# Kernel tuning notes

Measured on AMD Instinct MI355X. Metric: run time of the kernel, lower is better.

The kernel has to match this reference:

```python
import jax, jax.numpy as jnp
import numpy as np

FEAT_DIM = 2048
HID = 256
N = 1024
NUM_CLASSES = 16
BN_EPS = 1e-5


def _batchnorm(x, gamma, beta):
    # training-mode BatchNorm1d: per-batch mean, biased variance
    m = x.mean(axis=0)
    v = x.var(axis=0)
    return gamma * (x - m) / jnp.sqrt(v + BN_EPS) + beta


def setup_inputs() -> dict:
    key = jax.random.key(0)
    ks = jax.random.split(key, 12)
    s1 = 1.0 / np.sqrt(FEAT_DIM)
    s2 = 1.0 / np.sqrt(HID)
    s3 = 1.0 / np.sqrt(2 * HID)
    return {
        "features": jax.random.normal(ks[0], (N, FEAT_DIM), dtype=jnp.float32),
        "labels": jax.random.randint(ks[1], (N,), 0, NUM_CLASSES, dtype=jnp.int32),
        # semantic disentangler
        "W1": jax.random.normal(ks[2], (FEAT_DIM, HID), dtype=jnp.float32) * s1,
        "b1": jnp.zeros((HID,), jnp.float32),
        "g1": jnp.ones((HID,), jnp.float32),
        "bt1": jnp.zeros((HID,), jnp.float32),
        "W2": jax.random.normal(ks[3], (HID, HID), dtype=jnp.float32) * s2,
        "b2": jnp.zeros((HID,), jnp.float32),
        "g2": jnp.ones((HID,), jnp.float32),
        "bt2": jnp.zeros((HID,), jnp.float32),
        # edge network: Linear(2H -> H), Linear(H -> 1)
        "We1": jax.random.normal(ks[4], (2 * HID, HID), dtype=jnp.float32) * s3,
        "bwe1": jnp.zeros((HID,), jnp.float32),
        "We2": jax.random.normal(ks[5], (HID, 1), dtype=jnp.float32) * s2,
        "bwe2": jnp.zeros((1,), jnp.float32),
    }


def reference(features, labels, W1, b1, g1, bt1, W2, b2, g2, bt2,
              We1, bwe1, We2, bwe2):
    # semantic disentangler: (Linear -> BN -> ReLU) x2
    h = jax.nn.relu(_batchnorm(features @ W1 + b1, g1, bt1))
    di = jax.nn.relu(_batchnorm(h @ W2 + b2, g2, bt2))  # [N, H]

    # EdgeNetwork all-pairs: Linear on concat([f_i, f_j]) splits into two GEMMs
    hi = di @ We1[:HID]   # [N, H] contribution of node i (first half of concat)
    hj = di @ We1[HID:]   # [N, H] contribution of node j (second half)
    pair = jax.nn.relu(hi[:, None, :] + hj[None, :, :] + bwe1)  # [N, N, H]
    logits = pair @ We2[:, 0] + bwe2[0]                          # [N, N]
    same_label = labels[:, None] == labels[None, :]
    off_diag = ~jnp.eye(N, dtype=bool)
    edge_weights = jnp.where(same_label & off_diag,
                             jax.nn.sigmoid(logits), 0.0)        # [N, N]

    # update_node_features: f_i + sum_j w_ij f_j / sum_j w_ij (if wsum > 0)
    weighted_sum = edge_weights @ di                 # [N, H] (w_ii == 0)
    wsum = edge_weights.sum(axis=1, keepdims=True)   # [N, 1]
    denom = jnp.where(wsum > 0, wsum, 1.0)
    updated = di + jnp.where(wsum > 0, weighted_sum / denom, 0.0)
    return updated
```

## Files before the change

kernel.cpp:

```cpp
#include <hip/hip_runtime.h>
#include <math.h>

#define N_PTS 1024
#define HID   256
#define FEAT  2048

typedef short bf16x8 __attribute__((ext_vector_type(8)));
typedef float f32x4  __attribute__((ext_vector_type(4)));

__device__ inline ushort f2bf(float f) {
    union { float f; unsigned u; } v; v.f = f;
    unsigned r = v.u + 0x7fff + ((v.u >> 16) & 1);
    return (ushort)(r >> 16);
}

__global__ __launch_bounds__(256) void gemm_mfma(
    const float* __restrict__ A, const float* __restrict__ B,
    float* __restrict__ C, int lda, int ldb, int ldc, int kchunk)
{
    __shared__ ushort As[64 * 72];
    __shared__ ushort Bs[64 * 72];
    const int tid  = threadIdx.x;
    const int lane = tid & 63;
    const int wave = tid >> 6;
    const int wy = wave >> 1, wx = wave & 1;
    const int quad = lane >> 4, l16 = lane & 15;
    const int mBase = blockIdx.y * 64;
    const int nBase = blockIdx.x * 64;
    const int kBeg  = blockIdx.z * kchunk;

    f32x4 acc[2][2] = {};

    for (int ks = kBeg; ks < kBeg + kchunk; ks += 64) {
        #pragma unroll
        for (int p = 0; p < 4; p++) {
            const int c  = p * 256 + tid;
            const int r  = c >> 4;
            const int cq = c & 15;
            float4 av = *(const float4*)&A[(size_t)(mBase + r) * lda + ks + cq * 4];
            ushort4 ao;
            ao.x = f2bf(av.x); ao.y = f2bf(av.y);
            ao.z = f2bf(av.z); ao.w = f2bf(av.w);
            *(ushort4*)&As[r * 72 + cq * 4] = ao;
            float4 bv = *(const float4*)&B[(size_t)(ks + r) * ldb + nBase + cq * 4];
            Bs[(cq * 4 + 0) * 72 + r] = f2bf(bv.x);
            Bs[(cq * 4 + 1) * 72 + r] = f2bf(bv.y);
            Bs[(cq * 4 + 2) * 72 + r] = f2bf(bv.z);
            Bs[(cq * 4 + 3) * 72 + r] = f2bf(bv.w);
        }
        __syncthreads();
        #pragma unroll
        for (int kt = 0; kt < 64; kt += 32) {
            bf16x8 af[2], bfr[2];
            #pragma unroll
            for (int mi = 0; mi < 2; mi++)
                af[mi] = *(bf16x8*)&As[(wy * 32 + mi * 16 + l16) * 72 + kt + quad * 8];
            #pragma unroll
            for (int ni = 0; ni < 2; ni++)
                bfr[ni] = *(bf16x8*)&Bs[(wx * 32 + ni * 16 + l16) * 72 + kt + quad * 8];
            #pragma unroll
            for (int mi = 0; mi < 2; mi++)
                #pragma unroll
                for (int ni = 0; ni < 2; ni++)
                    acc[mi][ni] = __builtin_amdgcn_mfma_f32_16x16x32_bf16(
                        af[mi], bfr[ni], acc[mi][ni], 0, 0, 0);
        }
        __syncthreads();
    }
    #pragma unroll
    for (int mi = 0; mi < 2; mi++)
        #pragma unroll
        for (int ni = 0; ni < 2; ni++)
            #pragma unroll
            for (int e = 0; e < 4; e++) {
                const int gm = mBase + wy * 32 + mi * 16 + quad * 4 + e;
                const int gn = nBase + wx * 32 + ni * 16 + l16;
                unsafeAtomicAdd(&C[(size_t)gm * ldc + gn], acc[mi][ni][e]);
            }
}

__global__ __launch_bounds__(256) void colstats(
    const float* __restrict__ X, float* __restrict__ sum,
    float* __restrict__ sq, int rowsPerBlock)
{
    const int c = threadIdx.x;
    const int r0 = blockIdx.x * rowsPerBlock;
    float s = 0.f, q = 0.f;
    for (int r = r0; r < r0 + rowsPerBlock; ++r) {
        float v = X[r * HID + c];
        s += v;
        q = fmaf(v, v, q);
    }
    unsafeAtomicAdd(&sum[c], s);
    unsafeAtomicAdd(&sq[c], q);
}

__global__ __launch_bounds__(256) void bn_relu(
    const float* __restrict__ X, const float* __restrict__ sum,
    const float* __restrict__ sq, const float* __restrict__ g,
    const float* __restrict__ bt, float* __restrict__ Y)
{
    const int idx = blockIdx.x * 256 + threadIdx.x;
    const int cq = (idx & 63) * 4;
    float4 x = ((const float4*)X)[idx];
    float xv[4] = {x.x, x.y, x.z, x.w};
    float o[4];
    #pragma unroll
    for (int e = 0; e < 4; e++) {
        const int c = cq + e;
        float m   = sum[c] * (1.f / 1024.f);
        float var = fmaf(-m, m, sq[c] * (1.f / 1024.f));
        float rstd = rsqrtf(var + 1e-5f);
        o[e] = fmaxf(fmaf(g[c] * rstd, xv[e] - m, bt[c]), 0.f);
    }
    ((float4*)Y)[idx] = make_float4(o[0], o[1], o[2], o[3]);
}

__global__ __launch_bounds__(256) void pair_update(
    const float* __restrict__ di, const float* __restrict__ hi,
    const float* __restrict__ hj, const float* __restrict__ bwe1,
    const float* __restrict__ We2, const float* __restrict__ bwe2,
    const int* __restrict__ labels, float* __restrict__ out)
{
    __shared__ int   slab[N_PTS];
    __shared__ float sacc[4][HID];
    __shared__ float swsum[4];
    const int i = blockIdx.x;
    const int tid = threadIdx.x;
    const int lane = tid & 63;
    const int wave = tid >> 6;

    for (int t = tid; t < N_PTS; t += 256) slab[t] = labels[t];
    __syncthreads();

    const int myLab = slab[i];
    float4 hv_i = ((const float4*)(hi + (size_t)i * HID))[lane];
    float4 bw   = ((const float4*)bwe1)[lane];
    float4 w2   = ((const float4*)We2)[lane];
    const float hb0 = hv_i.x + bw.x, hb1 = hv_i.y + bw.y;
    const float hb2 = hv_i.z + bw.z, hb3 = hv_i.w + bw.w;
    const float b2 = bwe2[0];

    float a0 = 0.f, a1 = 0.f, a2 = 0.f, a3 = 0.f, wsum = 0.f;

    for (int chunk = wave * 64; chunk < N_PTS; chunk += 256) {
        const int j = chunk + lane;
        const bool match = (slab[j] == myLab) && (j != i);
        unsigned long long mask = __ballot(match);
        while (mask) {
            const int bpos = __builtin_ctzll(mask);
            mask &= mask - 1;
            const int jj = chunk + bpos;
            float4 hv = ((const float4*)(hj + (size_t)jj * HID))[lane];
            float p = fmaxf(hb0 + hv.x, 0.f) * w2.x
                    + fmaxf(hb1 + hv.y, 0.f) * w2.y
                    + fmaxf(hb2 + hv.z, 0.f) * w2.z
                    + fmaxf(hb3 + hv.w, 0.f) * w2.w;
            #pragma unroll
            for (int off = 1; off < 64; off <<= 1) p += __shfl_xor(p, off, 64);
            const float w = 1.f / (1.f + expf(-(p + b2)));
            float4 dv = ((const float4*)(di + (size_t)jj * HID))[lane];
            a0 = fmaf(w, dv.x, a0);
            a1 = fmaf(w, dv.y, a1);
            a2 = fmaf(w, dv.z, a2);
            a3 = fmaf(w, dv.w, a3);
            wsum += w;
        }
    }
    ((float4*)sacc[wave])[lane] = make_float4(a0, a1, a2, a3);
    if (lane == 0) swsum[wave] = wsum;
    __syncthreads();

    const float at = sacc[0][tid] + sacc[1][tid] + sacc[2][tid] + sacc[3][tid];
    const float wt = swsum[0] + swsum[1] + swsum[2] + swsum[3];
    const float dval = di[(size_t)i * HID + tid];
    out[(size_t)i * HID + tid] = dval + (wt > 0.f ? at / wt : 0.f);
}

extern "C" void kernel_launch(void* const* d_in, const int* in_sizes, int n_in,
                              void* d_out, int out_size, void* d_ws, size_t ws_size,
                              hipStream_t stream)
{
    const float* features = (const float*)d_in[0];
    const int*   labels   = (const int*)d_in[1];
    const float* W1   = (const float*)d_in[2];
    const float* g1   = (const float*)d_in[4];
    const float* bt1  = (const float*)d_in[5];
    const float* W2   = (const float*)d_in[6];
    const float* g2   = (const float*)d_in[8];
    const float* bt2  = (const float*)d_in[9];
    const float* We1  = (const float*)d_in[10];
    const float* bwe1 = (const float*)d_in[11];
    const float* We2  = (const float*)d_in[12];
    const float* bwe2 = (const float*)d_in[13];
    float* out = (float*)d_out;

    float* ws    = (float*)d_ws;
    float* x1    = ws;
    float* x2    = ws + 262144;
    float* hi    = ws + 524288;
    float* hj    = ws + 786432;
    float* stats = ws + 1048576;
    float* h     = ws + 1049600;
    float* di    = ws + 1311744;

    hipMemsetAsync(d_ws, 0, 1049600 * sizeof(float), stream);

    dim3 blk(256);
    gemm_mfma<<<dim3(4, 16, 8), blk, 0, stream>>>(features, W1, x1,
                                                  FEAT, HID, HID, 256);
    colstats<<<256, blk, 0, stream>>>(x1, stats, stats + 256, 4);
    bn_relu<<<256, blk, 0, stream>>>(x1, stats, stats + 256, g1, bt1, h);
    gemm_mfma<<<dim3(4, 16, 4), blk, 0, stream>>>(h, W2, x2,
                                                  HID, HID, HID, 64);
    colstats<<<256, blk, 0, stream>>>(x2, stats + 512, stats + 768, 4);
    bn_relu<<<256, blk, 0, stream>>>(x2, stats + 512, stats + 768, g2, bt2, di);
    gemm_mfma<<<dim3(4, 16, 4), blk, 0, stream>>>(di, We1, hi,
                                                  HID, HID, HID, 64);
    gemm_mfma<<<dim3(4, 16, 4), blk, 0, stream>>>(di, We1 + HID * HID, hj,
                                                  HID, HID, HID, 64);
    pair_update<<<N_PTS, blk, 0, stream>>>(di, hi, hj, bwe1, We2, bwe2,
                                           labels, out);
}
```

Baseline: 162.1 us.

## Pre-convert operands to bf16, fuse BN into GEMM loads, merge edge GEMMs

Features and weights are converted to bf16 once in prep kernels, and the weights are transposed so the GEMM loads B with vector copies instead of scattered LDS stores. The separate bn_relu kernels are removed: the last colstats block computes scale and shift, and BN+ReLU is applied while loading A in the next GEMM and in pair_update. The two edge GEMMs are merged into one N=512 GEMM, and the memset is replaced by a prep kernel. pair_update processes two matching neighbours per iteration to overlap their loads and reductions. This adds extra prep kernels and recomputes BN inside pair_update for every neighbour.

```diff
diff --git a/kernel.cpp b/kernel.cpp
--- a/kernel.cpp
+++ b/kernel.cpp
@@ -14,9 +14,65 @@
     return (ushort)(r >> 16);
 }
 
-__global__ __launch_bounds__(256) void gemm_mfma(
-    const float* __restrict__ A, const float* __restrict__ B,
-    float* __restrict__ C, int lda, int ldb, int ldc, int kchunk)
+__global__ __launch_bounds__(256) void prep_a(
+    const float* __restrict__ feat, ushort* __restrict__ featbf,
+    float* __restrict__ zbase, float* __restrict__ statsz)
+{
+    const int b = blockIdx.x, tid = threadIdx.x;
+    if (b < 1024) {
+        const int base = b * 2048 + tid * 8;
+        float4 v0 = *(const float4*)&feat[base];
+        float4 v1 = *(const float4*)&feat[base + 4];
+        ushort4 o0, o1;
+        o0.x = f2bf(v0.x); o0.y = f2bf(v0.y); o0.z = f2bf(v0.z); o0.w = f2bf(v0.w);
+        o1.x = f2bf(v1.x); o1.y = f2bf(v1.y); o1.z = f2bf(v1.z); o1.w = f2bf(v1.w);
+        *(ushort4*)&featbf[base]     = o0;
+        *(ushort4*)&featbf[base + 4] = o1;
+    } else if (b < 2048) {
+        float4 z = make_float4(0.f, 0.f, 0.f, 0.f);
+        *(float4*)&zbase[(size_t)(b - 1024) * 1024 + tid * 4] = z;
+    } else {
+        for (int t = tid; t < 2560; t += 256) statsz[t] = 0.f;
+    }
+}
+
+__global__ __launch_bounds__(256) void prep_t(
+    const float* __restrict__ W1, const float* __restrict__ W2,
+    const float* __restrict__ We1, ushort* __restrict__ Wt1,
+    ushort* __restrict__ Wt2, ushort* __restrict__ Wt34)
+{
+    __shared__ ushort T[64 * 72];
+    const int b = blockIdx.x, tid = threadIdx.x;
+    const float* src; ushort* dst; int Kd, kt, nt;
+    if (b < 128)      { src = W1;  dst = Wt1;  Kd = 2048; kt = b >> 2;        nt = b & 3; }
+    else if (b < 144) { int q = b - 128; src = W2;  dst = Wt2;  Kd = 256; kt = q >> 2; nt = q & 3; }
+    else if (b < 160) { int q = b - 144; src = We1; dst = Wt34; Kd = 256; kt = q >> 2; nt = q & 3; }
+    else              { int q = b - 160; src = We1 + 256 * 256; dst = Wt34 + 256 * 256;
+                        Kd = 256; kt = q >> 2; nt = q & 3; }
+    const int k0 = kt * 64, n0 = nt * 64;
+    #pragma unroll
+    for (int p = 0; p < 4; p++) {
+        const int c = p * 256 + tid, r = c >> 4, q = c & 15;
+        float4 v = *(const float4*)&src[(size_t)(k0 + r) * 256 + n0 + q * 4];
+        T[(q * 4 + 0) * 72 + r] = f2bf(v.x);
+        T[(q * 4 + 1) * 72 + r] = f2bf(v.y);
+        T[(q * 4 + 2) * 72 + r] = f2bf(v.z);
+        T[(q * 4 + 3) * 72 + r] = f2bf(v.w);
+    }
+    __syncthreads();
+    #pragma unroll
+    for (int p = 0; p < 2; p++) {
+        const int c = p * 256 + tid, r = c >> 3, q = c & 7;
+        *(bf16x8*)&dst[(size_t)(n0 + r) * Kd + k0 + q * 8] = *(bf16x8*)&T[r * 72 + q * 8];
+    }
+}
+
+template<bool BN>
+__global__ __launch_bounds__(256) void gemm_bf(
+    const ushort* __restrict__ Abf, const float* __restrict__ Afp,
+    const float* __restrict__ scale, const float* __restrict__ shift,
+    const ushort* __restrict__ Bt, float* __restrict__ C,
+    int lda, int ldb, int ldc, int kchunk)
 {
     __shared__ ushort As[64 * 72];
     __shared__ ushort Bs[64 * 72];
@@ -32,21 +88,33 @@
     f32x4 acc[2][2] = {};
 
     for (int ks = kBeg; ks < kBeg + kchunk; ks += 64) {
+        if (BN) {
+            #pragma unroll
+            for (int p = 0; p < 4; p++) {
+                const int c = p * 256 + tid, r = c >> 4, q = c & 15;
+                float4 v  = *(const float4*)&Afp[(size_t)(mBase + r) * lda + ks + q * 4];
+                float4 sc = *(const float4*)&scale[ks + q * 4];
+                float4 sh = *(const float4*)&shift[ks + q * 4];
+                ushort4 o;
+                o.x = f2bf(fmaxf(fmaf(v.x, sc.x, sh.x), 0.f));
+                o.y = f2bf(fmaxf(fmaf(v.y, sc.y, sh.y), 0.f));
+                o.z = f2bf(fmaxf(fmaf(v.z, sc.z, sh.z), 0.f));
+                o.w = f2bf(fmaxf(fmaf(v.w, sc.w, sh.w), 0.f));
+                *(ushort4*)&As[r * 72 + q * 4] = o;
+            }
+        } else {
+            #pragma unroll
+            for (int p = 0; p < 2; p++) {
+                const int c = p * 256 + tid, r = c >> 3, q = c & 7;
+                *(bf16x8*)&As[r * 72 + q * 8] =
+                    *(const bf16x8*)&Abf[(size_t)(mBase + r) * lda + ks + q * 8];
+            }
+        }
         #pragma unroll
-        for (int p = 0; p < 4; p++) {
-            const int c  = p * 256 + tid;
-            const int r  = c >> 4;
-            const int cq = c & 15;
-            float4 av = *(const float4*)&A[(size_t)(mBase + r) * lda + ks + cq * 4];
-            ushort4 ao;
-            ao.x = f2bf(av.x); ao.y = f2bf(av.y);
-            ao.z = f2bf(av.z); ao.w = f2bf(av.w);
-            *(ushort4*)&As[r * 72 + cq * 4] = ao;
-            float4 bv = *(const float4*)&B[(size_t)(ks + r) * ldb + nBase + cq * 4];
-            Bs[(cq * 4 + 0) * 72 + r] = f2bf(bv.x);
-            Bs[(cq * 4 + 1) * 72 + r] = f2bf(bv.y);
-            Bs[(cq * 4 + 2) * 72 + r] = f2bf(bv.z);
-            Bs[(cq * 4 + 3) * 72 + r] = f2bf(bv.w);
+        for (int p = 0; p < 2; p++) {
+            const int c = p * 256 + tid, r = c >> 3, q = c & 7;
+            *(bf16x8*)&Bs[r * 72 + q * 8] =
+                *(const bf16x8*)&Bt[(size_t)(nBase + r) * ldb + ks + q * 8];
         }
         __syncthreads();
         #pragma unroll
@@ -79,48 +147,45 @@
             }
 }
 
-__global__ __launch_bounds__(256) void colstats(
-    const float* __restrict__ X, float* __restrict__ sum,
-    float* __restrict__ sq, int rowsPerBlock)
+__global__ __launch_bounds__(256) void colstats_fin(
+    const float* __restrict__ X, float* __restrict__ sum, float* __restrict__ sq,
+    unsigned* __restrict__ ticket, const float* __restrict__ g,
+    const float* __restrict__ bt, float* __restrict__ scale,
+    float* __restrict__ shift)
 {
     const int c = threadIdx.x;
-    const int r0 = blockIdx.x * rowsPerBlock;
+    const int r0 = blockIdx.x * 4;
     float s = 0.f, q = 0.f;
-    for (int r = r0; r < r0 + rowsPerBlock; ++r) {
+    #pragma unroll
+    for (int r = r0; r < r0 + 4; ++r) {
         float v = X[r * HID + c];
         s += v;
         q = fmaf(v, v, q);
     }
     unsafeAtomicAdd(&sum[c], s);
     unsafeAtomicAdd(&sq[c], q);
-}
-
-__global__ __launch_bounds__(256) void bn_relu(
-    const float* __restrict__ X, const float* __restrict__ sum,
-    const float* __restrict__ sq, const float* __restrict__ g,
-    const float* __restrict__ bt, float* __restrict__ Y)
-{
-    const int idx = blockIdx.x * 256 + threadIdx.x;
-    const int cq = (idx & 63) * 4;
-    float4 x = ((const float4*)X)[idx];
-    float xv[4] = {x.x, x.y, x.z, x.w};
-    float o[4];
-    #pragma unroll
-    for (int e = 0; e < 4; e++) {
-        const int c = cq + e;
-        float m   = sum[c] * (1.f / 1024.f);
-        float var = fmaf(-m, m, sq[c] * (1.f / 1024.f));
-        float rstd = rsqrtf(var + 1e-5f);
-        o[e] = fmaxf(fmaf(g[c] * rstd, xv[e] - m, bt[c]), 0.f);
-    }
-    ((float4*)Y)[idx] = make_float4(o[0], o[1], o[2], o[3]);
+    __threadfence();
+    __syncthreads();
+    __shared__ int last;
+    if (c == 0) last = (atomicAdd(ticket, 1u) == 255u) ? 1 : 0;
+    __syncthreads();
+    if (last) {
+        float s2 = atomicAdd(&sum[c], 0.f);
+        float q2 = atomicAdd(&sq[c], 0.f);
+        float m   = s2 * (1.f / 1024.f);
+        float var = fmaf(-m, m, q2 * (1.f / 1024.f));
+        float sc  = g[c] * rsqrtf(var + 1e-5f);
+        scale[c] = sc;
+        shift[c] = fmaf(-sc, m, bt[c]);
+    }
 }
 
 __global__ __launch_bounds__(256) void pair_update(
-    const float* __restrict__ di, const float* __restrict__ hi,
-    const float* __restrict__ hj, const float* __restrict__ bwe1,
-    const float* __restrict__ We2, const float* __restrict__ bwe2,
-    const int* __restrict__ labels, float* __restrict__ out)
+    const float* __restrict__ x2, const float* __restrict__ hic,
+    const float* __restrict__ scale2, const float* __restrict__ shift2,
+    const float* __restrict__ bwe1, const float* __restrict__ We2,
+    const float* __restrict__ bwe2, const int* __restrict__ labels,
+    float* __restrict__ out)
 {
     __shared__ int   slab[N_PTS];
     __shared__ float sacc[4][HID];
@@ -134,9 +199,11 @@
     __syncthreads();
 
     const int myLab = slab[i];
-    float4 hv_i = ((const float4*)(hi + (size_t)i * HID))[lane];
+    float4 hv_i = *(const float4*)&hic[(size_t)i * 512 + lane * 4];
     float4 bw   = ((const float4*)bwe1)[lane];
     float4 w2   = ((const float4*)We2)[lane];
+    float4 sc   = ((const float4*)scale2)[lane];
+    float4 sh   = ((const float4*)shift2)[lane];
     const float hb0 = hv_i.x + bw.x, hb1 = hv_i.y + bw.y;
     const float hb2 = hv_i.z + bw.z, hb3 = hv_i.w + bw.w;
     const float b2 = bwe2[0];
@@ -148,23 +215,48 @@
         const bool match = (slab[j] == myLab) && (j != i);
         unsigned long long mask = __ballot(match);
         while (mask) {
-            const int bpos = __builtin_ctzll(mask);
+            const int b0 = __builtin_ctzll(mask);
             mask &= mask - 1;
-            const int jj = chunk + bpos;
-            float4 hv = ((const float4*)(hj + (size_t)jj * HID))[lane];
-            float p = fmaxf(hb0 + hv.x, 0.f) * w2.x
-                    + fmaxf(hb1 + hv.y, 0.f) * w2.y
-                    + fmaxf(hb2 + hv.z, 0.f) * w2.z
-                    + fmaxf(hb3 + hv.w, 0.f) * w2.w;
-            #pragma unroll
-            for (int off = 1; off < 64; off <<= 1) p += __shfl_xor(p, off, 64);
-            const float w = 1.f / (1.f + expf(-(p + b2)));
-            float4 dv = ((const float4*)(di + (size_t)jj * HID))[lane];
-            a0 = fmaf(w, dv.x, a0);
-            a1 = fmaf(w, dv.y, a1);
-            a2 = fmaf(w, dv.z, a2);
-            a3 = fmaf(w, dv.w, a3);
-            wsum += w;
+            const int jj0 = chunk + b0;
+            const bool dual = (mask != 0ull);
+            int jj1 = jj0;
+            if (dual) {
+                const int b1 = __builtin_ctzll(mask);
+                mask &= mask - 1;
+                jj1 = chunk + b1;
+            }
+            float4 hv0 = *(const float4*)&hic[(size_t)jj0 * 512 + 256 + lane * 4];
+            float4 hv1 = *(const float4*)&hic[(size_t)jj1 * 512 + 256 + lane * 4];
+            float p0 = fmaxf(hb0 + hv0.x, 0.f) * w2.x
+                     + fmaxf(hb1 + hv0.y, 0.f) * w2.y
+                     + fmaxf(hb2 + hv0.z, 0.f) * w2.z
+                     + fmaxf(hb3 + hv0.w, 0.f) * w2.w;
+            float p1 = fmaxf(hb0 + hv1.x, 0.f) * w2.x
+                     + fmaxf(hb1 + hv1.y, 0.f) * w2.y
+                     + fmaxf(hb2 + hv1.z, 0.f) * w2.z
+                     + fmaxf(hb3 + hv1.w, 0.f) * w2.w;
+            #pragma unroll
+            for (int off = 1; off < 64; off <<= 1) {
+                p0 += __shfl_xor(p0, off, 64);
+                p1 += __shfl_xor(p1, off, 64);
+            }
+            const float w0 = 1.f / (1.f + expf(-(p0 + b2)));
+            const float w1 = dual ? 1.f / (1.f + expf(-(p1 + b2))) : 0.f;
+            float4 xv0 = *(const float4*)&x2[(size_t)jj0 * HID + lane * 4];
+            float4 xv1 = *(const float4*)&x2[(size_t)jj1 * HID + lane * 4];
+            float d00 = fmaxf(fmaf(xv0.x, sc.x, sh.x), 0.f);
+            float d01 = fmaxf(fmaf(xv0.y, sc.y, sh.y), 0.f);
+            float d02 = fmaxf(fmaf(xv0.z, sc.z, sh.z), 0.f);
+            float d03 = fmaxf(fmaf(xv0.w, sc.w, sh.w), 0.f);
+            float d10 = fmaxf(fmaf(xv1.x, sc.x, sh.x), 0.f);
+            float d11 = fmaxf(fmaf(xv1.y, sc.y, sh.y), 0.f);
+            float d12 = fmaxf(fmaf(xv1.z, sc.z, sh.z), 0.f);
+            float d13 = fmaxf(fmaf(xv1.w, sc.w, sh.w), 0.f);
+            a0 = fmaf(w0, d00, fmaf(w1, d10, a0));
+            a1 = fmaf(w0, d01, fmaf(w1, d11, a1));
+            a2 = fmaf(w0, d02, fmaf(w1, d12, a2));
+            a3 = fmaf(w0, d03, fmaf(w1, d13, a3));
+            wsum += w0 + w1;
         }
     }
     ((float4*)sacc[wave])[lane] = make_float4(a0, a1, a2, a3);
@@ -173,8 +265,8 @@
 
     const float at = sacc[0][tid] + sacc[1][tid] + sacc[2][tid] + sacc[3][tid];
     const float wt = swsum[0] + swsum[1] + swsum[2] + swsum[3];
-    const float dval = di[(size_t)i * HID + tid];
-    out[(size_t)i * HID + tid] = dval + (wt > 0.f ? at / wt : 0.f);
+    const float di_i = fmaxf(fmaf(x2[(size_t)i * HID + tid], scale2[tid], shift2[tid]), 0.f);
+    out[(size_t)i * HID + tid] = di_i + (wt > 0.f ? at / wt : 0.f);
 }
 
 extern "C" void kernel_launch(void* const* d_in, const int* in_sizes, int n_in,
@@ -195,30 +287,34 @@
     const float* bwe2 = (const float*)d_in[13];
     float* out = (float*)d_out;
 
-    float* ws    = (float*)d_ws;
-    float* x1    = ws;
-    float* x2    = ws + 262144;
-    float* hi    = ws + 524288;
-    float* hj    = ws + 786432;
-    float* stats = ws + 1048576;
-    float* h     = ws + 1049600;
-    float* di    = ws + 1311744;
-
-    hipMemsetAsync(d_ws, 0, 1049600 * sizeof(float), stream);
+    float* ws = (float*)d_ws;
+    float*  x1     = ws;
+    float*  x2     = ws + 262144;
+    float*  hic    = ws + 524288;
+    float*  stats  = ws + 1048576;
+    float*  sum1 = stats,        *sq1 = stats + 256;
+    float*  scale1 = stats + 512, *shift1 = stats + 768;
+    float*  sum2 = stats + 1024, *sq2 = stats + 1280;
+    float*  scale2 = stats + 1536, *shift2 = stats + 1792;
+    unsigned* tickets = (unsigned*)(stats + 2048);
+    ushort* featbf = (ushort*)(ws + 1051136);
+    ushort* Wt1    = (ushort*)(ws + 2099712);
+    ushort* Wt2    = (ushort*)(ws + 2361856);
+    ushort* Wt34   = (ushort*)(ws + 2394624);
 
     dim3 blk(256);
-    gemm_mfma<<<dim3(4, 16, 8), blk, 0, stream>>>(features, W1, x1,
-                                                  FEAT, HID, HID, 256);
-    colstats<<<256, blk, 0, stream>>>(x1, stats, stats + 256, 4);
-    bn_relu<<<256, blk, 0, stream>>>(x1, stats, stats + 256, g1, bt1, h);
-    gemm_mfma<<<dim3(4, 16, 4), blk, 0, stream>>>(h, W2, x2,
-                                                  HID, HID, HID, 64);
-    colstats<<<256, blk, 0, stream>>>(x2, stats + 512, stats + 768, 4);
-    bn_relu<<<256, blk, 0, stream>>>(x2, stats + 512, stats + 768, g2, bt2, di);
-    gemm_mfma<<<dim3(4, 16, 4), blk, 0, stream>>>(di, We1, hi,
-                                                  HID, HID, HID, 64);
-    gemm_mfma<<<dim3(4, 16, 4), blk, 0, stream>>>(di, We1 + HID * HID, hj,
-                                                  HID, HID, HID, 64);
-    pair_update<<<N_PTS, blk, 0, stream>>>(di, hi, hj, bwe1, We2, bwe2,
-                                           labels, out);
-}
+    prep_a<<<2049, blk, 0, stream>>>(features, featbf, ws, stats);
+    prep_t<<<176, blk, 0, stream>>>(W1, W2, We1, Wt1, Wt2, Wt34);
+    gemm_bf<false><<<dim3(4, 16, 8), blk, 0, stream>>>(
+        featbf, nullptr, nullptr, nullptr, Wt1, x1, FEAT, FEAT, HID, 256);
+    colstats_fin<<<256, blk, 0, stream>>>(x1, sum1, sq1, tickets, g1, bt1,
+                                          scale1, shift1);
+    gemm_bf<true><<<dim3(4, 16, 4), blk, 0, stream>>>(
+        nullptr, x1, scale1, shift1, Wt2, x2, HID, HID, HID, 64);
+    colstats_fin<<<256, blk, 0, stream>>>(x2, sum2, sq2, tickets + 1, g2, bt2,
+                                          scale2, shift2);
+    gemm_bf<true><<<dim3(8, 16, 4), blk, 0, stream>>>(
+        nullptr, x2, scale2, shift2, Wt34, hic, HID, HID, 512, 64);
+    pair_update<<<N_PTS, blk, 0, stream>>>(x2, hic, scale2, shift2,
+                                           bwe1, We2, bwe2, labels, out);
+}
```

After: 168.7 us. 1.04x slower.
